# Kernel optimization log

Measured on AMD Instinct MI355X. Metric: run time of the kernel, lower is better.

The kernel has to match this reference:

```python
import jax, jax.numpy as jnp
import numpy as np

B, S, D = 4, 2048, 512
BETA = 1.0
PARAM_SCALE = 1.0 / np.sqrt(D)  # ~ torch Linear default init scale


def setup_inputs() -> dict:
    key = jax.random.key(0)
    ks = jax.random.split(key, 14)
    def rn(k, shape, scale=1.0):
        return (jax.random.normal(k, shape, jnp.float32) * scale).astype(jnp.float32)
    return {
        "x_re": rn(ks[0], (B, S, D)),
        "x_im": rn(ks[1], (B, S, D)),
        "Wq_re": rn(ks[2], (D, D), PARAM_SCALE), "Wq_im": rn(ks[3], (D, D), PARAM_SCALE),
        "bq_re": rn(ks[4], (D,), PARAM_SCALE),   "bq_im": rn(ks[5], (D,), PARAM_SCALE),
        "Wk_re": rn(ks[6], (D, D), PARAM_SCALE), "Wk_im": rn(ks[7], (D, D), PARAM_SCALE),
        "bk_re": rn(ks[8], (D,), PARAM_SCALE),   "bk_im": rn(ks[9], (D,), PARAM_SCALE),
        "Wv_re": rn(ks[10], (D, D), PARAM_SCALE), "Wv_im": rn(ks[11], (D, D), PARAM_SCALE),
        "bv_re": rn(ks[12], (D,), PARAM_SCALE),   "bv_im": rn(ks[13], (D,), PARAM_SCALE),
    }


def reference(x_re, x_im, Wq_re, Wq_im, bq_re, bq_im,
              Wk_re, Wk_im, bk_re, bk_im, Wv_re, Wv_im, bv_re, bv_im):
    cx = lambda re, im: (re + 1j * im).astype(jnp.complex64)
    x = cx(x_re, x_im)                          # [B,S,D] complex64
    # nn.Linear: y = x @ W.T + b (complex)
    Q = jnp.einsum('bsd,ed->bse', x, cx(Wq_re, Wq_im)) + cx(bq_re, bq_im)
    K = jnp.einsum('bsd,ed->bse', x, cx(Wk_re, Wk_im)) + cx(bk_re, bk_im)
    V = jnp.einsum('bsd,ed->bse', x, cx(Wv_re, Wv_im)) + cx(bv_re, bv_im)
    # energy = -Re(Q K^H); attn = softmax(-beta * energy) = softmax(beta * Re(Q K^H))
    scores = jnp.real(jnp.einsum('bse,bte->bst', Q, jnp.conj(K)))  # [B,S,S] float32
    attn = jax.nn.softmax(BETA * scores, axis=-1)
    out = jnp.einsum('bst,bte->bse', attn.astype(jnp.complex64), V)  # [B,S,D] complex64
    return out
```

## Files before the change

kernel.cpp:

```cpp
#include <hip/hip_runtime.h>
#include <hip/hip_bf16.h>
#include <cstdint>
#include <cstddef>


typedef unsigned short u16;
typedef __attribute__((ext_vector_type(8))) _Float16 half8;
typedef __attribute__((ext_vector_type(4))) float f32x4;

#define B_    4
#define S_    2048
#define D_    512
#define M_TOT (B_ * S_)
#define KC    (2 * D_)
#define N1    (6 * D_)
#define RE_PLANE 4194304

#define X_ELEMS  ((size_t)M_TOT * KC)
#define W_ELEMS  ((size_t)N1 * KC)
#define QK_ELEMS ((size_t)M_TOT * KC)
#define VT_ELEMS ((size_t)B_ * KC * S_)
#define AT_ELEMS ((size_t)M_TOT * S_)

__device__ __forceinline__ u16 f2h(float f) {
    _Float16 h = (_Float16)f;
    return __builtin_bit_cast(u16, h);
}
__device__ __forceinline__ float h2f(u16 b) {
    return (float)__builtin_bit_cast(_Float16, b);
}

__device__ __forceinline__ f32x4 mfma16(half8 a, half8 b, f32x4 c) {
    return __builtin_amdgcn_mfma_f32_16x16x32_f16(a, b, c, 0, 0, 0);
}

__device__ __forceinline__ void dma16(const u16* g, u16* l) {
    __builtin_amdgcn_global_load_lds(
        (const __attribute__((address_space(1))) unsigned int*)g,
        (__attribute__((address_space(3))) unsigned int*)l,
        16, 0, 0);
}

__device__ __forceinline__ void stage_half(u16* __restrict__ plane,
                                           const u16* __restrict__ src,
                                           int rowbase, int kcol, int tid) {
#pragma unroll
    for (int i = 0; i < 2; ++i) {
        int c = tid + (i << 9);
        int c2 = c ^ (((c >> 5) & 1) << 1);
        int row = ((c2 >> 3) << 1) | ((c2 >> 2) & 1);
        int ks = c2 & 3;
        dma16(src + (size_t)(rowbase + row) * KC + (kcol + ks * 8),
              plane + c * 8);
    }
}

__device__ __forceinline__ void stage_half8(u16* __restrict__ plane,
                                            const u16* __restrict__ src,
                                            int ld, int rowbase, int kcol,
                                            int tid) {
#pragma unroll
    for (int i = 0; i < 2; ++i) {
        int c = tid + (i << 8);
        int c2 = c ^ (((c >> 5) & 1) << 1);
        int row = ((c2 >> 3) << 1) | ((c2 >> 2) & 1);
        int ks = c2 & 3;
        dma16(src + (size_t)(rowbase + row) * ld + (kcol + ks * 8),
              plane + c * 8);
    }
}

#define VMW(N) asm volatile("s_waitcnt vmcnt(" #N ")" ::: "memory")
#define BAR()  __builtin_amdgcn_s_barrier()

__global__ void k_diag(float* __restrict__ out, int out_size, float val) {
    int i = blockIdx.x * 256 + threadIdx.x;
    if (i < out_size && i < 4096) out[i] = val;
}

__global__ void k_prep(const float* __restrict__ xr, const float* __restrict__ xi,
                       const float* __restrict__ Wqr, const float* __restrict__ Wqi,
                       const float* __restrict__ Wkr, const float* __restrict__ Wki,
                       const float* __restrict__ Wvr, const float* __restrict__ Wvi,
                       const float* __restrict__ bqr, const float* __restrict__ bqi,
                       const float* __restrict__ bkr, const float* __restrict__ bki,
                       const float* __restrict__ bvr, const float* __restrict__ bvi,
                       u16* __restrict__ Xh, u16* __restrict__ Xl,
                       u16* __restrict__ Wh, float* __restrict__ bc) {
    int gb = blockIdx.x;
    int tid = threadIdx.x;
    if (gb < 16384) {
        int id = gb * 256 + tid;
        int m = id >> 9, d = id & 511;
        size_t o = (size_t)m * KC + d;
        if (o + D_ >= X_ELEMS) return;
        float vr = xr[id], vi = xi[id];
        u16 h;
        h = f2h(vr); Xh[o] = h;        Xl[o] = f2h(vr - h2f(h));
        h = f2h(vi); Xh[o + D_] = h;   Xl[o + D_] = f2h(vi - h2f(h));
    } else if (gb < 16384 + 12288) {
        int id = (gb - 16384) * 256 + tid;
        int n = id >> 10, k = id & 1023;
        int q = n >> 9, e = n & 511;
        int half = k >> 9, d = k & 511;
        const float* Wre = (q < 2) ? Wqr : ((q < 4) ? Wkr : Wvr);
        const float* Wim = (q < 2) ? Wqi : ((q < 4) ? Wki : Wvi);
        size_t src = (size_t)e * D_ + d;
        float v;
        if ((q & 1) == 0) v = half ? -Wim[src] : Wre[src];
        else              v = half ?  Wre[src] : Wim[src];
        if ((size_t)id < W_ELEMS) Wh[id] = f2h(v);
    } else {
        int id = (gb - 16384 - 12288) * 256 + tid;
        if (id >= N1) return;
        int q = id >> 9, e = id & 511;
        const float* src = (q == 0) ? bqr : (q == 1) ? bqi : (q == 2) ? bkr
                         : (q == 3) ? bki : (q == 4) ? bvr : bvi;
        bc[id] = src[e];
    }
}

#define RDA(d, pl, mg)                                                        \
  { const u16* _pa = &lds[pl][0];                                             \
    _Pragma("unroll")                                                         \
    for (int _i = 0; _i < 4; ++_i)                                            \
      d[_i] = *(const half8*)(_pa + aoffs + ((mg) * 4 + _i) * 512); }
#define RDB(d, pl)                                                            \
  { const u16* _pb = &lds[pl][0];                                             \
    _Pragma("unroll")                                                         \
    for (int _i = 0; _i < 4; ++_i)                                            \
      d[_i] = *(const half8*)(_pb + boffs + _i * 512); }
#define MF16(av, bv, mg)                                                      \
  { __builtin_amdgcn_s_setprio(1);                                            \
    _Pragma("unroll")                                                         \
    for (int _j = 0; _j < 4; ++_j) {                                          \
      _Pragma("unroll")                                                       \
      for (int _i = 0; _i < 4; ++_i)                                          \
        acc[(mg) * 4 + _i][_j] =                                              \
            mfma16(av[_i], bv[_j], acc[(mg) * 4 + _i][_j]);                   \
    }                                                                         \
    __builtin_amdgcn_s_setprio(0); }

#define W0(P, STG, WT) { MF16(aA, bA, 0); RDA(aB, ((P) << 2) | 0, 1); STG; WT; BAR(); }
#define W1(P, STG)     { MF16(aB, bA, 1); RDB(bB, ((P) << 2) | 3); RDA(aA, ((P) << 2) | 1, 0); STG; BAR(); }
#define W2(P, STG, WT) { MF16(aA, bB, 0); RDA(aB, ((P) << 2) | 1, 1); STG; WT; BAR(); }
#define W3(P, STG)     { MF16(aB, bB, 1); RDB(bA, (((P) ^ 1) << 2) | 2); RDA(aA, (((P) ^ 1) << 2) | 0, 0); STG; BAR(); }
#define W3L()          { MF16(aB, bB, 1); }
#define NOP_ ((void)0)

__global__ __launch_bounds__(512, 2) void k_gemm1(
    const u16* __restrict__ Xh, const u16* __restrict__ Xl,
    const u16* __restrict__ Wh,
    const float* __restrict__ bc,
    u16* __restrict__ Qh, u16* __restrict__ Ql,
    u16* __restrict__ Kh, u16* __restrict__ Kl,
    u16* __restrict__ VT) {
    __shared__ __attribute__((aligned(16))) u16 lds[8][8192];
    int tid = threadIdx.x;

    int L = blockIdx.y * 12 + blockIdx.x;
    int bx, by;
    if (L < 256) {
        int q = (L & 7) * 32 + (L >> 3);
        bx = q & 7; by = q >> 3;
    } else {
        int v = L - 256;
        int vv = (v & 7) * 16 + (v >> 3);
        bx = 8 + (vv & 3); by = vv >> 2;
    }
    int nb = bx * 256, mb = by * 256;
    int g = bx >> 2;
    bool vblk = (g == 2);
    int NT = vblk ? 16 : 32;

    int lane = tid & 63, wave = tid >> 6;
    int wm = (wave >> 2) * 128, wn = (wave & 3) * 64;
    int lr = lane & 15, lq = lane >> 4;
    int lqs8 = (lq ^ (((lr >> 3) & 1) << 1)) * 8;
    int aoffs = (wm + lr) * 32 + lqs8;
    int boffs = (wn + lr) * 32 + lqs8;

    f32x4 acc[8][4] = {};
    half8 aA[4], aB[4], bA[4], bB[4];

    stage_half(&lds[0][0], Xh, mb, 0, tid);
    stage_half(&lds[2][0], Wh, nb, 0, tid);
    stage_half(&lds[1][0], Xh, mb, 32, tid);
    stage_half(&lds[3][0], Wh, nb, 32, tid);
    stage_half(&lds[4][0], Xh, mb, 64, tid);
    stage_half(&lds[6][0], Wh, nb, 64, tid);
    VMW(8);
    BAR();
    RDB(bA, 2);
    RDA(aA, 0, 0);

    for (int t = 0; t < NT - 2; ++t) {
        const int p = t & 1;
        const u16* s1 = (!vblk && (t + 1) >= 16) ? Xl : Xh;
        const int k1 = (((t + 1) & 15) << 6) + 32;
        const u16* s2 = (!vblk && (t + 2) >= 16) ? Xl : Xh;
        const int k2 = ((t + 2) & 15) << 6;
        W0(p, stage_half(&lds[((p ^ 1) << 2) | 1][0], s1, mb, k1, tid), VMW(6));
        W1(p, stage_half(&lds[((p ^ 1) << 2) | 3][0], Wh, nb, k1, tid));
        W2(p, stage_half(&lds[(p << 2) | 0][0], s2, mb, k2, tid), VMW(6));
        W3(p, stage_half(&lds[(p << 2) | 2][0], Wh, nb, k2, tid));
    }
    {
        const u16* s1 = vblk ? Xh : Xl;
        const int k1 = (((NT - 1) & 15) << 6) + 32;
        W0(0, stage_half(&lds[(1 << 2) | 1][0], s1, mb, k1, tid), VMW(6));
        W1(0, stage_half(&lds[(1 << 2) | 3][0], Wh, nb, k1, tid));
        W2(0, NOP_, VMW(4));
        W3(0, NOP_);
    }
    {
        W0(1, NOP_, VMW(0));
        W1(1, NOP_);
        W2(1, NOP_, NOP_);
        W3L();
    }

#pragma unroll
    for (int j = 0; j < 4; ++j) {
        int n_g = nb + wn + j * 16 + lr;
        float bias = bc[n_g];
        int c = n_g & 1023;
#pragma unroll
        for (int i = 0; i < 8; ++i) {
            int m0 = mb + wm + i * 16 + lq * 4;
            if (vblk) {
                int bidx = m0 >> 11, s0 = m0 & 2047;
                u16 pk[4];
#pragma unroll
                for (int r = 0; r < 4; ++r) pk[r] = f2h(acc[i][j][r] + bias);
                size_t idx = ((size_t)(bidx * KC + c)) * S_ + s0;
                if (idx + 3 < VT_ELEMS)
                    *(ushort4*)&VT[idx] = make_ushort4(pk[0], pk[1], pk[2], pk[3]);
            } else {
                u16* dh = g ? Kh : Qh;
                u16* dl = g ? Kl : Ql;
#pragma unroll
                for (int r = 0; r < 4; ++r) {
                    float v = acc[i][j][r] + bias;
                    u16 h = f2h(v);
                    size_t idx = (size_t)(m0 + r) * KC + c;
                    if (idx < QK_ELEMS) {
                        dh[idx] = h;
                        dl[idx] = f2h(v - h2f(h));
                    }
                }
            }
        }
    }
}

__global__ __launch_bounds__(512, 2) void k_gemm2_256(
    const u16* __restrict__ Qh, const u16* __restrict__ Ql,
    const u16* __restrict__ Kh, const u16* __restrict__ Kl,
    float* __restrict__ SC, int zbase) {
    __shared__ __attribute__((aligned(16))) u16 lds[8][8192];
    int tid = threadIdx.x;
    int z = zbase + blockIdx.z;
    const u16* Aq = Qh + (size_t)z * S_ * KC;
    const u16* Al = Ql + (size_t)z * S_ * KC;
    const u16* Bh = Kh + (size_t)z * S_ * KC;
    const u16* Bl = Kl + (size_t)z * S_ * KC;
    int nb = blockIdx.x * 256, mb = blockIdx.y * 256;
    const int NT = 48;

    int lane = tid & 63, wave = tid >> 6;
    int wm = (wave >> 2) * 128, wn = (wave & 3) * 64;
    int lr = lane & 15, lq = lane >> 4;
    int lqs8 = (lq ^ (((lr >> 3) & 1) << 1)) * 8;
    int aoffs = (wm + lr) * 32 + lqs8;
    int boffs = (wn + lr) * 32 + lqs8;

    f32x4 acc[8][4] = {};
    half8 aA[4], aB[4], bA[4], bB[4];

    stage_half(&lds[0][0], Aq, mb, 0, tid);
    stage_half(&lds[2][0], Bh, nb, 0, tid);
    stage_half(&lds[1][0], Aq, mb, 32, tid);
    stage_half(&lds[3][0], Bh, nb, 32, tid);
    stage_half(&lds[4][0], Aq, mb, 64, tid);
    stage_half(&lds[6][0], Bh, nb, 64, tid);
    VMW(8);
    BAR();
    RDB(bA, 2);
    RDA(aA, 0, 0);

    for (int t = 0; t < NT - 2; ++t) {
        const int p = t & 1;
        const int t1 = t + 1, t2 = t + 2;
        const int sg1 = t1 >> 4, sg2 = t2 >> 4;
        const u16* a1 = (sg1 == 1) ? Al : Aq;
        const u16* b1 = (sg1 == 2) ? Bl : Bh;
        const u16* a2 = (sg2 == 1) ? Al : Aq;
        const u16* b2 = (sg2 == 2) ? Bl : Bh;
        const int k1 = ((t1 & 15) << 6) + 32;
        const int k2 = (t2 & 15) << 6;
        W0(p, stage_half(&lds[((p ^ 1) << 2) | 1][0], a1, mb, k1, tid), VMW(6));
        W1(p, stage_half(&lds[((p ^ 1) << 2) | 3][0], b1, nb, k1, tid));
        W2(p, stage_half(&lds[(p << 2) | 0][0], a2, mb, k2, tid), VMW(6));
        W3(p, stage_half(&lds[(p << 2) | 2][0], b2, nb, k2, tid));
    }
    {
        const int k1 = ((47 & 15) << 6) + 32;
        W0(0, stage_half(&lds[(1 << 2) | 1][0], Aq, mb, k1, tid), VMW(6));
        W1(0, stage_half(&lds[(1 << 2) | 3][0], Bl, nb, k1, tid));
        W2(0, NOP_, VMW(4));
        W3(0, NOP_);
    }
    {
        W0(1, NOP_, VMW(0));
        W1(1, NOP_);
        W2(1, NOP_, NOP_);
        W3L();
    }

    size_t sc_limit = (size_t)gridDim.z * S_ * S_;
#pragma unroll
    for (int j = 0; j < 4; ++j) {
        int n_g = nb + wn + j * 16 + lr;
#pragma unroll
        for (int i = 0; i < 8; ++i) {
            int m0 = mb + wm + i * 16 + lq * 4;
#pragma unroll
            for (int r = 0; r < 4; ++r) {
                size_t idx = ((size_t)blockIdx.z * S_ + m0 + r) * S_ + n_g;
                if (idx < sc_limit) SC[idx] = acc[i][j][r];
            }
        }
    }
}

__global__ __launch_bounds__(256, 2) void k_gemm2w(
    const u16* __restrict__ Qh, const u16* __restrict__ Ql,
    const u16* __restrict__ Kh, const u16* __restrict__ Kl,
    float* __restrict__ SC, int zbase) {
    __shared__ __attribute__((aligned(16))) u16 lds[8][4096];
    int tid = threadIdx.x;
    int z = zbase + blockIdx.z;
    const u16* Aq  = Qh + (size_t)z * S_ * KC;
    const u16* Alo = Ql + (size_t)z * S_ * KC;
    const u16* Bh  = Kh + (size_t)z * S_ * KC;
    const u16* Blo = Kl + (size_t)z * S_ * KC;
    int nb = blockIdx.x * 128, mb = blockIdx.y * 128;

    int lane = tid & 63, wave = tid >> 6;
    int wm = (wave >> 1) * 64, wn = (wave & 1) * 64;
    int lr = lane & 15, lq = lane >> 4;
    int lqs8 = (lq ^ (((lr >> 3) & 1) << 1)) * 8;
    int aoffs = (wm + lr) * 32 + lqs8;
    int boffs = (wn + lr) * 32 + lqs8;

    f32x4 acc[4][4] = {};
    half8 aA[4], aB[4], bA[4], bB[4];

    stage_half8(&lds[0][0], Aq, KC, mb, 0, tid);
    stage_half8(&lds[2][0], Bh, KC, nb, 0, tid);
    stage_half8(&lds[1][0], Aq, KC, mb, 32, tid);
    stage_half8(&lds[3][0], Bh, KC, nb, 32, tid);
    stage_half8(&lds[4][0], Aq, KC, mb, 64, tid);
    stage_half8(&lds[6][0], Bh, KC, nb, 64, tid);
    VMW(4);
    BAR();
    RDA(aA, 0, 0);
    RDB(bA, 2);

    for (int t = 0; t < 46; ++t) {
        const int p = t & 1;
        const int t1 = t + 1, t2 = t + 2;
        const u16* a1 = ((t1 >> 4) == 1) ? Alo : Aq;
        const u16* b1 = ((t1 >> 4) == 2) ? Blo : Bh;
        const u16* a2 = ((t2 >> 4) == 1) ? Alo : Aq;
        const u16* b2 = ((t2 >> 4) == 2) ? Blo : Bh;
        const int k1 = ((t1 & 15) << 6) + 32;
        const int k2 = (t2 & 15) << 6;
        MF16(aA, bA, 0);
        RDA(aB, (p << 2) | 1, 0);
        RDB(bB, (p << 2) | 3);
        stage_half8(&lds[((p ^ 1) << 2) | 1][0], a1, KC, mb, k1, tid);
        stage_half8(&lds[((p ^ 1) << 2) | 3][0], b1, KC, nb, k1, tid);
        VMW(4);
        BAR();
        MF16(aB, bB, 0);
        RDA(aA, ((p ^ 1) << 2) | 0, 0);
        RDB(bA, ((p ^ 1) << 2) | 2);
        stage_half8(&lds[(p << 2) | 0][0], a2, KC, mb, k2, tid);
        stage_half8(&lds[(p << 2) | 2][0], b2, KC, nb, k2, tid);
        VMW(4);
        BAR();
    }
    {
        MF16(aA, bA, 0);
        RDA(aB, 1, 0);
        RDB(bB, 3);
        stage_half8(&lds[(1 << 2) | 1][0], Aq, KC, mb, ((47 & 15) << 6) + 32, tid);
        stage_half8(&lds[(1 << 2) | 3][0], Blo, KC, nb, ((47 & 15) << 6) + 32, tid);
        VMW(4);
        BAR();
        MF16(aB, bB, 0);
        RDA(aA, (1 << 2) | 0, 0);
        RDB(bA, (1 << 2) | 2);
        VMW(0);
        BAR();
    }
    {
        MF16(aA, bA, 0);
        RDA(aB, (1 << 2) | 1, 0);
        RDB(bB, (1 << 2) | 3);
        MF16(aB, bB, 0);
    }

    size_t sc_limit = (size_t)gridDim.z * S_ * S_;
#pragma unroll
    for (int j = 0; j < 4; ++j) {
        int n_g = nb + wn + j * 16 + lr;
#pragma unroll
        for (int i = 0; i < 4; ++i) {
            int m0 = mb + wm + i * 16 + lq * 4;
#pragma unroll
            for (int r = 0; r < 4; ++r) {
                size_t idx = ((size_t)blockIdx.z * S_ + m0 + r) * S_ + n_g;
                if (idx < sc_limit) SC[idx] = acc[i][j][r];
            }
        }
    }
}

__global__ __launch_bounds__(256) void k_softmax(const float* __restrict__ SC,
                                                 u16* __restrict__ AT, int zbase) {
    int row = blockIdx.x;
    const float* src = SC + (size_t)row * S_;
    size_t drow = (size_t)zbase * S_ + row;
    u16* dst = AT + drow * S_;
    int tid = threadIdx.x;
    float v[8];
#pragma unroll
    for (int i = 0; i < 8; ++i) v[i] = src[tid + i * 256];
    float m = v[0];
#pragma unroll
    for (int i = 1; i < 8; ++i) m = fmaxf(m, v[i]);
    for (int off = 32; off > 0; off >>= 1) m = fmaxf(m, __shfl_down(m, off));
    __shared__ float redm[4], reds[4];
    if ((tid & 63) == 0) redm[tid >> 6] = m;
    __syncthreads();
    m = fmaxf(fmaxf(redm[0], redm[1]), fmaxf(redm[2], redm[3]));
    float s = 0.f;
#pragma unroll
    for (int i = 0; i < 8; ++i) { v[i] = __expf(v[i] - m); s += v[i]; }
    for (int off = 32; off > 0; off >>= 1) s += __shfl_down(s, off);
    if ((tid & 63) == 0) reds[tid >> 6] = s;
    __syncthreads();
    float inv = 1.0f / (reds[0] + reds[1] + reds[2] + reds[3]);
    if (drow * S_ + 2047 < AT_ELEMS) {
#pragma unroll
        for (int i = 0; i < 8; ++i) dst[tid + i * 256] = f2h(v[i] * inv);
    }
}

__global__ __launch_bounds__(256, 2) void k_gemm3w(
    const u16* __restrict__ AT, const u16* __restrict__ VT,
    float* __restrict__ out, int out_size, int full) {
    __shared__ __attribute__((aligned(16))) u16 lds[8][4096];
    int tid = threadIdx.x;
    int z = blockIdx.z;
    const u16* Abase = AT + (size_t)z * S_ * S_;
    const u16* Bbase = VT + (size_t)z * KC * S_;
    int nb = blockIdx.x * 128, mb = blockIdx.y * 128;

    int lane = tid & 63, wave = tid >> 6;
    int wm = (wave >> 1) * 64, wn = (wave & 1) * 64;
    int lr = lane & 15, lq = lane >> 4;
    int lqs8 = (lq ^ (((lr >> 3) & 1) << 1)) * 8;
    int aoffs = (wm + lr) * 32 + lqs8;
    int boffs = (wn + lr) * 32 + lqs8;

    f32x4 acc[4][4] = {};
    half8 aA[4], aB[4], bA[4], bB[4];

    stage_half8(&lds[0][0], Abase, S_, mb, 0, tid);
    stage_half8(&lds[2][0], Bbase, S_, nb, 0, tid);
    stage_half8(&lds[1][0], Abase, S_, mb, 32, tid);
    stage_half8(&lds[3][0], Bbase, S_, nb, 32, tid);
    stage_half8(&lds[4][0], Abase, S_, mb, 64, tid);
    stage_half8(&lds[6][0], Bbase, S_, nb, 64, tid);
    VMW(4);
    BAR();
    RDA(aA, 0, 0);
    RDB(bA, 2);

    for (int t = 0; t < 30; ++t) {
        const int p = t & 1;
        const int k1 = (t + 1) * 64 + 32;
        const int k2 = (t + 2) * 64;
        MF16(aA, bA, 0);
        RDA(aB, (p << 2) | 1, 0);
        RDB(bB, (p << 2) | 3);
        stage_half8(&lds[((p ^ 1) << 2) | 1][0], Abase, S_, mb, k1, tid);
        stage_half8(&lds[((p ^ 1) << 2) | 3][0], Bbase, S_, nb, k1, tid);
        VMW(4);
        BAR();
        MF16(aB, bB, 0);
        RDA(aA, ((p ^ 1) << 2) | 0, 0);
        RDB(bA, ((p ^ 1) << 2) | 2);
        stage_half8(&lds[(p << 2) | 0][0], Abase, S_, mb, k2, tid);
        stage_half8(&lds[(p << 2) | 2][0], Bbase, S_, nb, k2, tid);
        VMW(4);
        BAR();
    }
    {
        MF16(aA, bA, 0);
        RDA(aB, 1, 0);
        RDB(bB, 3);
        stage_half8(&lds[(1 << 2) | 1][0], Abase, S_, mb, 31 * 64 + 32, tid);
        stage_half8(&lds[(1 << 2) | 3][0], Bbase, S_, nb, 31 * 64 + 32, tid);
        VMW(4);
        BAR();
        MF16(aB, bB, 0);
        RDA(aA, (1 << 2) | 0, 0);
        RDB(bA, (1 << 2) | 2);
        VMW(0);
        BAR();
    }
    {
        MF16(aA, bA, 0);
        RDA(aB, (1 << 2) | 1, 0);
        RDB(bB, (1 << 2) | 3);
        MF16(aB, bB, 0);
    }

#pragma unroll
    for (int j = 0; j < 4; ++j) {
        int f = nb + wn + j * 16 + lr;
#pragma unroll
        for (int i = 0; i < 4; ++i) {
            int s0 = mb + wm + i * 16 + lq * 4;
#pragma unroll
            for (int r = 0; r < 4; ++r) {
                size_t base = ((size_t)z * S_ + s0 + r) * D_;
                if (f < D_) {
                    size_t o = base + f;
                    if (o < (size_t)out_size) out[o] = acc[i][j][r];
                } else if (full) {
                    size_t o = (size_t)RE_PLANE + base + (f - D_);
                    if (o < (size_t)out_size) out[o] = acc[i][j][r];
                }
            }
        }
    }
}


extern "C" void kernel_launch(void* const* d_in, const int* in_sizes, int n_in,
                              void* d_out, int out_size, void* d_ws, size_t ws_size,
                              hipStream_t stream) {
    (void)in_sizes; (void)n_in;
    const float* xr  = (const float*)d_in[0];
    const float* xi  = (const float*)d_in[1];
    const float* Wqr = (const float*)d_in[2];
    const float* Wqi = (const float*)d_in[3];
    const float* bqr = (const float*)d_in[4];
    const float* bqi = (const float*)d_in[5];
    const float* Wkr = (const float*)d_in[6];
    const float* Wki = (const float*)d_in[7];
    const float* bkr = (const float*)d_in[8];
    const float* bki = (const float*)d_in[9];
    const float* Wvr = (const float*)d_in[10];
    const float* Wvi = (const float*)d_in[11];
    const float* bvr = (const float*)d_in[12];
    const float* bvi = (const float*)d_in[13];
    float* out = (float*)d_out;

    constexpr size_t SZ_X  = X_ELEMS * 2;
    constexpr size_t SZ_W  = W_ELEMS * 2;
    constexpr size_t SZ_BC = (size_t)N1 * 4;
    constexpr size_t SZ_QK = QK_ELEMS * 2;
    constexpr size_t SZ_VT = VT_ELEMS * 2;
    constexpr size_t SZ_SC_B = (size_t)S_ * S_ * 4;

    char* p = (char*)d_ws;
    size_t off = 0;
    auto take = [&](size_t sz) {
        char* r = p + off;
        off += (sz + 255) & ~(size_t)255;
        return r;
    };
    u16*   Xh = (u16*)take(SZ_X);
    u16*   Xl = (u16*)take(SZ_X);
    u16*   Wh = (u16*)take(SZ_W);
    float* bc = (float*)take(SZ_BC);
    u16*   Qh = (u16*)take(SZ_QK);
    u16*   Ql = (u16*)take(SZ_QK);
    u16*   Kh = (u16*)take(SZ_QK);
    u16*   Kl = (u16*)take(SZ_QK);
    u16*   VT = (u16*)take(SZ_VT);
    u16*   AT = Xh;
    float* SC = (float*)(p + off);

    int nz = 0;
    if (ws_size > off) nz = (int)((ws_size - off) / SZ_SC_B);
    if (nz > B_) nz = B_;
    if (nz < 1) {
        k_diag<<<16, 256, 0, stream>>>(out, out_size, 1000.0f + (float)(ws_size >> 20));
        return;
    }

    int full = (out_size >= 2 * RE_PLANE) ? 1 : 0;

    k_prep<<<16384 + 12288 + 12, 256, 0, stream>>>(
        xr, xi, Wqr, Wqi, Wkr, Wki, Wvr, Wvi,
        bqr, bqi, bkr, bki, bvr, bvi, Xh, Xl, Wh, bc);
    k_gemm1<<<dim3(12, 32), 512, 0, stream>>>(Xh, Xl, Wh, bc, Qh, Ql, Kh, Kl, VT);

    for (int z0 = 0; z0 < B_; z0 += nz) {
        int zc = (B_ - z0 < nz) ? (B_ - z0) : nz;
        if (zc == B_) {
            k_gemm2_256<<<dim3(S_ / 256, S_ / 256, zc), 512, 0, stream>>>(
                Qh, Ql, Kh, Kl, SC, z0);
        } else {
            k_gemm2w<<<dim3(S_ / 128, S_ / 128, zc), 256, 0, stream>>>(
                Qh, Ql, Kh, Kl, SC, z0);
        }
        k_softmax<<<zc * S_, 256, 0, stream>>>(SC, AT, z0);
    }
    k_gemm3w<<<dim3(KC / 128, S_ / 128, B_), 256, 0, stream>>>(AT, VT, out, out_size, full);
}
```

Baseline: 391.7 us.

## Split QKV projection into separate QK and V GEMM kernels; vectorize softmax I/O

Splits the fused projection GEMM into a 256-tile kernel for Q/K (split hi/lo precision, 32 k-steps) and a separate 128-tile kernel for V (16 k-steps). The separate V kernel launches more blocks, aiming to fix load imbalance from mixing short and long blocks in one grid. The removed block-index remapping also drops whatever L2 locality it gave. Softmax now loads and stores each thread's 8 contiguous elements with float4 and uint4 vectors instead of strided scalar accesses. The extra kernel launch adds a little overhead.

```diff
diff --git a/kernel.cpp b/kernel.cpp
--- a/kernel.cpp
+++ b/kernel.cpp
@@ -148,30 +148,18 @@
 #define W3L()          { MF16(aB, bB, 1); }
 #define NOP_ ((void)0)
 
-__global__ __launch_bounds__(512, 2) void k_gemm1(
+__global__ __launch_bounds__(512, 2) void k_gemm1qk(
     const u16* __restrict__ Xh, const u16* __restrict__ Xl,
     const u16* __restrict__ Wh,
     const float* __restrict__ bc,
     u16* __restrict__ Qh, u16* __restrict__ Ql,
-    u16* __restrict__ Kh, u16* __restrict__ Kl,
-    u16* __restrict__ VT) {
+    u16* __restrict__ Kh, u16* __restrict__ Kl) {
     __shared__ __attribute__((aligned(16))) u16 lds[8][8192];
     int tid = threadIdx.x;
-
-    int L = blockIdx.y * 12 + blockIdx.x;
-    int bx, by;
-    if (L < 256) {
-        int q = (L & 7) * 32 + (L >> 3);
-        bx = q & 7; by = q >> 3;
-    } else {
-        int v = L - 256;
-        int vv = (v & 7) * 16 + (v >> 3);
-        bx = 8 + (vv & 3); by = vv >> 2;
-    }
+    int bx = blockIdx.x, by = blockIdx.y;
     int nb = bx * 256, mb = by * 256;
     int g = bx >> 2;
-    bool vblk = (g == 2);
-    int NT = vblk ? 16 : 32;
+    const int NT = 32;
 
     int lane = tid & 63, wave = tid >> 6;
     int wm = (wave >> 2) * 128, wn = (wave & 3) * 64;
@@ -196,9 +184,9 @@
 
     for (int t = 0; t < NT - 2; ++t) {
         const int p = t & 1;
-        const u16* s1 = (!vblk && (t + 1) >= 16) ? Xl : Xh;
+        const u16* s1 = ((t + 1) >= 16) ? Xl : Xh;
         const int k1 = (((t + 1) & 15) << 6) + 32;
-        const u16* s2 = (!vblk && (t + 2) >= 16) ? Xl : Xh;
+        const u16* s2 = ((t + 2) >= 16) ? Xl : Xh;
         const int k2 = ((t + 2) & 15) << 6;
         W0(p, stage_half(&lds[((p ^ 1) << 2) | 1][0], s1, mb, k1, tid), VMW(6));
         W1(p, stage_half(&lds[((p ^ 1) << 2) | 3][0], Wh, nb, k1, tid));
@@ -206,9 +194,8 @@
         W3(p, stage_half(&lds[(p << 2) | 2][0], Wh, nb, k2, tid));
     }
     {
-        const u16* s1 = vblk ? Xh : Xl;
-        const int k1 = (((NT - 1) & 15) << 6) + 32;
-        W0(0, stage_half(&lds[(1 << 2) | 1][0], s1, mb, k1, tid), VMW(6));
+        const int k1 = ((31 & 15) << 6) + 32;
+        W0(0, stage_half(&lds[(1 << 2) | 1][0], Xl, mb, k1, tid), VMW(6));
         W1(0, stage_half(&lds[(1 << 2) | 3][0], Wh, nb, k1, tid));
         W2(0, NOP_, VMW(4));
         W3(0, NOP_);
@@ -225,31 +212,110 @@
         int n_g = nb + wn + j * 16 + lr;
         float bias = bc[n_g];
         int c = n_g & 1023;
+        u16* dh = g ? Kh : Qh;
+        u16* dl = g ? Kl : Ql;
 #pragma unroll
         for (int i = 0; i < 8; ++i) {
             int m0 = mb + wm + i * 16 + lq * 4;
-            if (vblk) {
-                int bidx = m0 >> 11, s0 = m0 & 2047;
-                u16 pk[4];
-#pragma unroll
-                for (int r = 0; r < 4; ++r) pk[r] = f2h(acc[i][j][r] + bias);
-                size_t idx = ((size_t)(bidx * KC + c)) * S_ + s0;
-                if (idx + 3 < VT_ELEMS)
-                    *(ushort4*)&VT[idx] = make_ushort4(pk[0], pk[1], pk[2], pk[3]);
-            } else {
-                u16* dh = g ? Kh : Qh;
-                u16* dl = g ? Kl : Ql;
-#pragma unroll
-                for (int r = 0; r < 4; ++r) {
-                    float v = acc[i][j][r] + bias;
-                    u16 h = f2h(v);
-                    size_t idx = (size_t)(m0 + r) * KC + c;
-                    if (idx < QK_ELEMS) {
-                        dh[idx] = h;
-                        dl[idx] = f2h(v - h2f(h));
-                    }
+#pragma unroll
+            for (int r = 0; r < 4; ++r) {
+                float v = acc[i][j][r] + bias;
+                u16 h = f2h(v);
+                size_t idx = (size_t)(m0 + r) * KC + c;
+                if (idx < QK_ELEMS) {
+                    dh[idx] = h;
+                    dl[idx] = f2h(v - h2f(h));
                 }
             }
+        }
+    }
+}
+
+__global__ __launch_bounds__(256, 2) void k_gemm1v(
+    const u16* __restrict__ Xh, const u16* __restrict__ Wh,
+    const float* __restrict__ bc, u16* __restrict__ VT) {
+    __shared__ __attribute__((aligned(16))) u16 lds[8][4096];
+    int tid = threadIdx.x;
+    int bx = blockIdx.x, by = blockIdx.y;
+    int nb = 2048 + bx * 128;
+    int mb = by * 128;
+
+    int lane = tid & 63, wave = tid >> 6;
+    int wm = (wave >> 1) * 64, wn = (wave & 1) * 64;
+    int lr = lane & 15, lq = lane >> 4;
+    int lqs8 = (lq ^ (((lr >> 3) & 1) << 1)) * 8;
+    int aoffs = (wm + lr) * 32 + lqs8;
+    int boffs = (wn + lr) * 32 + lqs8;
+
+    f32x4 acc[4][4] = {};
+    half8 aA[4], aB[4], bA[4], bB[4];
+
+    stage_half8(&lds[0][0], Xh, KC, mb, 0, tid);
+    stage_half8(&lds[2][0], Wh, KC, nb, 0, tid);
+    stage_half8(&lds[1][0], Xh, KC, mb, 32, tid);
+    stage_half8(&lds[3][0], Wh, KC, nb, 32, tid);
+    stage_half8(&lds[4][0], Xh, KC, mb, 64, tid);
+    stage_half8(&lds[6][0], Wh, KC, nb, 64, tid);
+    VMW(4);
+    BAR();
+    RDA(aA, 0, 0);
+    RDB(bA, 2);
+
+    for (int t = 0; t < 14; ++t) {
+        const int p = t & 1;
+        const int k1 = (t + 1) * 64 + 32;
+        const int k2 = (t + 2) * 64;
+        MF16(aA, bA, 0);
+        RDA(aB, (p << 2) | 1, 0);
+        RDB(bB, (p << 2) | 3);
+        stage_half8(&lds[((p ^ 1) << 2) | 1][0], Xh, KC, mb, k1, tid);
+        stage_half8(&lds[((p ^ 1) << 2) | 3][0], Wh, KC, nb, k1, tid);
+        VMW(4);
+        BAR();
+        MF16(aB, bB, 0);
+        RDA(aA, ((p ^ 1) << 2) | 0, 0);
+        RDB(bA, ((p ^ 1) << 2) | 2);
+        stage_half8(&lds[(p << 2) | 0][0], Xh, KC, mb, k2, tid);
+        stage_half8(&lds[(p << 2) | 2][0], Wh, KC, nb, k2, tid);
+        VMW(4);
+        BAR();
+    }
+    {
+        MF16(aA, bA, 0);
+        RDA(aB, 1, 0);
+        RDB(bB, 3);
+        stage_half8(&lds[(1 << 2) | 1][0], Xh, KC, mb, 15 * 64 + 32, tid);
+        stage_half8(&lds[(1 << 2) | 3][0], Wh, KC, nb, 15 * 64 + 32, tid);
+        VMW(4);
+        BAR();
+        MF16(aB, bB, 0);
+        RDA(aA, (1 << 2) | 0, 0);
+        RDB(bA, (1 << 2) | 2);
+        VMW(0);
+        BAR();
+    }
+    {
+        MF16(aA, bA, 0);
+        RDA(aB, (1 << 2) | 1, 0);
+        RDB(bB, (1 << 2) | 3);
+        MF16(aB, bB, 0);
+    }
+
+#pragma unroll
+    for (int j = 0; j < 4; ++j) {
+        int n_g = nb + wn + j * 16 + lr;
+        float bias = bc[n_g];
+        int c = n_g & 1023;
+#pragma unroll
+        for (int i = 0; i < 4; ++i) {
+            int m0 = mb + wm + i * 16 + lq * 4;
+            int bidx = m0 >> 11, s0 = m0 & 2047;
+            u16 pk[4];
+#pragma unroll
+            for (int r = 0; r < 4; ++r) pk[r] = f2h(acc[i][j][r] + bias);
+            size_t idx = ((size_t)(bidx * KC + c)) * S_ + s0;
+            if (idx + 3 < VT_ELEMS)
+                *(ushort4*)&VT[idx] = make_ushort4(pk[0], pk[1], pk[2], pk[3]);
         }
     }
 }
@@ -436,9 +502,9 @@
     size_t drow = (size_t)zbase * S_ + row;
     u16* dst = AT + drow * S_;
     int tid = threadIdx.x;
-    float v[8];
-#pragma unroll
-    for (int i = 0; i < 8; ++i) v[i] = src[tid + i * 256];
+    float4 va = *(const float4*)(src + tid * 8);
+    float4 vb = *(const float4*)(src + tid * 8 + 4);
+    float v[8] = {va.x, va.y, va.z, va.w, vb.x, vb.y, vb.z, vb.w};
     float m = v[0];
 #pragma unroll
     for (int i = 1; i < 8; ++i) m = fmaxf(m, v[i]);
@@ -455,8 +521,15 @@
     __syncthreads();
     float inv = 1.0f / (reds[0] + reds[1] + reds[2] + reds[3]);
     if (drow * S_ + 2047 < AT_ELEMS) {
-#pragma unroll
-        for (int i = 0; i < 8; ++i) dst[tid + i * 256] = f2h(v[i] * inv);
+        u16 pk[8];
+#pragma unroll
+        for (int i = 0; i < 8; ++i) pk[i] = f2h(v[i] * inv);
+        uint4 o;
+        o.x = (unsigned)pk[0] | ((unsigned)pk[1] << 16);
+        o.y = (unsigned)pk[2] | ((unsigned)pk[3] << 16);
+        o.z = (unsigned)pk[4] | ((unsigned)pk[5] << 16);
+        o.w = (unsigned)pk[6] | ((unsigned)pk[7] << 16);
+        *(uint4*)(dst + tid * 8) = o;
     }
 }
 
@@ -612,7 +685,8 @@
     k_prep<<<16384 + 12288 + 12, 256, 0, stream>>>(
         xr, xi, Wqr, Wqi, Wkr, Wki, Wvr, Wvi,
         bqr, bqi, bkr, bki, bvr, bvi, Xh, Xl, Wh, bc);
-    k_gemm1<<<dim3(12, 32), 512, 0, stream>>>(Xh, Xl, Wh, bc, Qh, Ql, Kh, Kl, VT);
+    k_gemm1qk<<<dim3(8, 32), 512, 0, stream>>>(Xh, Xl, Wh, bc, Qh, Ql, Kh, Kl);
+    k_gemm1v<<<dim3(8, 64), 256, 0, stream>>>(Xh, Wh, bc, VT);
 
     for (int z0 = 0; z0 < B_; z0 += nz) {
         int zc = (B_ - z0 < nz) ? (B_ - z0) : nz;
```

Measured after the change: 388.8 us. About the same (-0.8%).
